# Optimization experiments

Measured on AMD Instinct MI355X. Metric: run time of the kernel, lower is better.

## Reference

```python
import jax, jax.numpy as jnp
import numpy as np

B, N, D, H, O, K, N_USER, C = 1, 4096, 64, 4, 64, 2, 4000, 2


def setup_inputs() -> dict:
    key = jax.random.key(0)
    ks = jax.random.split(key, 7)
    h = jax.random.normal(ks[0], (B, N, D), jnp.float32)
    # dense 0/1 adjacency per heterogeneous kind, with self-loops so no row is empty
    adj = jax.random.randint(ks[1], (K, B, N, N), 0, 2).astype(jnp.float32)
    hadj = jnp.maximum(adj, jnp.eye(N, dtype=jnp.float32))
    s = 1.0 / np.sqrt(D).astype(np.float32)
    w = jax.random.normal(ks[2], (K, H, D, O), jnp.float32) * s
    a_src = jax.random.normal(ks[3], (K, H, O, 1), jnp.float32) * (1.0 / np.sqrt(O).astype(np.float32))
    a_dst = jax.random.normal(ks[4], (K, H, O, 1), jnp.float32) * (1.0 / np.sqrt(O).astype(np.float32))
    fc_w = jax.random.normal(ks[5], (C, O * K), jnp.float32) * (1.0 / np.sqrt(O * K).astype(np.float32))
    fc_b = jnp.zeros((C,), jnp.float32)
    return {"h": h, "hadj": hadj, "w": w, "a_src": a_src, "a_dst": a_dst, "fc_w": fc_w, "fc_b": fc_b}


def _gat(h, adj, w_k, a_src_k, a_dst_k):
    # h: (B,N,D); adj: (B,N,N); w_k: (H,D,O); a_*: (H,O,1)
    h_prime = jnp.einsum('bnf,hfo->bhno', h, w_k)          # (B,H,N,O)
    t = jnp.tanh(h_prime)
    attn_src = jnp.einsum('bhno,hoi->bhni', t, a_src_k)    # (B,H,N,1)
    attn_dst = jnp.einsum('bhno,hoi->bhni', t, a_dst_k)    # (B,H,N,1)
    attn = attn_src + jnp.swapaxes(attn_dst, -1, -2)       # (B,H,N,N) broadcast add
    attn = jnp.where(attn >= 0, attn, 0.2 * attn)          # LeakyReLU(0.2)
    attn = jnp.where(adj[:, None] > 0, attn, -jnp.inf)     # dense mask
    attn = jax.nn.softmax(attn, axis=-1)                   # dropout is a no-op in eval
    out = jnp.einsum('bhnm,bhmo->bhno', attn, h_prime)     # (B,H,N,O)
    return out.mean(axis=1)                                # mean over heads -> (B,N,O)


def reference(h, hadj, w, a_src, a_dst, fc_w, fc_b):
    embs = []
    for k in range(K):  # small fixed loop over heterogeneous node kinds
        x = _gat(h, hadj[k], w[k], a_src[k], a_dst[k])
        embs.append(x[:, :N_USER])
    type_aware = jnp.concatenate(embs, axis=-1)            # (B, N_USER, K*O)
    logits = type_aware @ fc_w.T + fc_b                    # (B, N_USER, C)
    return jax.nn.log_softmax(logits, axis=-1)
```

## Files before the change

### kernel.cpp

```cpp
#include <hip/hip_runtime.h>
#include <math.h>

constexpr int KK = 2;
constexpr int HH = 4;
constexpr int NN = 4096;
constexpr int DD = 64;
constexpr int OO = 64;
constexpr int NU = 4000;
constexpr int CC = 2;
constexpr int JSPLIT = 8;
constexpr int JCHUNK = NN / JSPLIT;
constexpr float LOG2E = 1.44269504088896340736f;

typedef float vf4 __attribute__((ext_vector_type(4)));
typedef float vf2 __attribute__((ext_vector_type(2)));

__device__ __forceinline__ float fexp2(float x) {
#if __has_builtin(__builtin_amdgcn_exp2f)
  return __builtin_amdgcn_exp2f(x);
#else
  return exp2f(x);
#endif
}
__device__ __forceinline__ float frcp(float x) {
#if __has_builtin(__builtin_amdgcn_rcpf)
  return __builtin_amdgcn_rcpf(x);
#else
  return 1.0f / x;
#endif
}
__device__ __forceinline__ float ftanh(float x) {
  float e = fexp2(x * (2.0f * LOG2E));
  return 1.0f - 2.0f * frcp(e + 1.0f);
}

__global__ __launch_bounds__(256) void gat_phase1(
    const float* __restrict__ hsrc, const float* __restrict__ w,
    const float* __restrict__ a_src, const float* __restrict__ a_dst,
    const float* __restrict__ fc_w,
    float* __restrict__ Ap, float* __restrict__ A5p,
    float* __restrict__ Bp, float* __restrict__ B5p,
    float* __restrict__ G0p, float* __restrict__ G1p) {
  const int kh = blockIdx.y;
  const int k = kh >> 2;
  const int i0 = blockIdx.x * 64;
  const int tid = threadIdx.x;

  __shared__ float h_s[DD][68];
  __shared__ float w_s[DD][OO];
  __shared__ float part[4][64][17];

  {
    const vf4* wp = (const vf4*)(w + (size_t)kh * DD * OO);
    vf4* ws4 = (vf4*)w_s;
    for (int t = tid; t < DD * OO / 4; t += 256) ws4[t] = wp[t];
  }
  for (int t = tid; t < 1024; t += 256) {
    const int row = t >> 4;
    const int f4 = (t & 15) * 4;
    vf4 v = *(const vf4*)(hsrc + (size_t)(i0 + row) * DD + f4);
    h_s[f4 + 0][row] = v.x;
    h_s[f4 + 1][row] = v.y;
    h_s[f4 + 2][row] = v.z;
    h_s[f4 + 3][row] = v.w;
  }
  __syncthreads();

  const int og = tid & 15;
  const int rg = tid >> 4;
  const int o0 = og * 4;
  const int r0 = rg * 4;

  float hp[4][4];
#pragma unroll
  for (int j = 0; j < 4; ++j)
#pragma unroll
    for (int u = 0; u < 4; ++u) hp[j][u] = 0.0f;

#pragma unroll 8
  for (int f = 0; f < DD; ++f) {
    vf4 hv = *(const vf4*)&h_s[f][r0];
    vf4 wv = *(const vf4*)&w_s[f][o0];
    hp[0][0] = fmaf(hv.x, wv.x, hp[0][0]);
    hp[0][1] = fmaf(hv.x, wv.y, hp[0][1]);
    hp[0][2] = fmaf(hv.x, wv.z, hp[0][2]);
    hp[0][3] = fmaf(hv.x, wv.w, hp[0][3]);
    hp[1][0] = fmaf(hv.y, wv.x, hp[1][0]);
    hp[1][1] = fmaf(hv.y, wv.y, hp[1][1]);
    hp[1][2] = fmaf(hv.y, wv.z, hp[1][2]);
    hp[1][3] = fmaf(hv.y, wv.w, hp[1][3]);
    hp[2][0] = fmaf(hv.z, wv.x, hp[2][0]);
    hp[2][1] = fmaf(hv.z, wv.y, hp[2][1]);
    hp[2][2] = fmaf(hv.z, wv.z, hp[2][2]);
    hp[2][3] = fmaf(hv.z, wv.w, hp[2][3]);
    hp[3][0] = fmaf(hv.w, wv.x, hp[3][0]);
    hp[3][1] = fmaf(hv.w, wv.y, hp[3][1]);
    hp[3][2] = fmaf(hv.w, wv.z, hp[3][2]);
    hp[3][3] = fmaf(hv.w, wv.w, hp[3][3]);
  }

  float as[4], ad[4], f0[4], f1[4];
#pragma unroll
  for (int u = 0; u < 4; ++u) {
    as[u] = a_src[kh * OO + o0 + u];
    ad[u] = a_dst[kh * OO + o0 + u];
    f0[u] = fc_w[0 * (KK * OO) + k * OO + o0 + u];
    f1[u] = fc_w[1 * (KK * OO) + k * OO + o0 + u];
  }

#pragma unroll
  for (int j = 0; j < 4; ++j) {
    float sp = 0.0f, dp = 0.0f, g0 = 0.0f, g1 = 0.0f;
#pragma unroll
    for (int u = 0; u < 4; ++u) {
      float v = hp[j][u];
      float t = ftanh(v);
      sp = fmaf(t, as[u], sp);
      dp = fmaf(t, ad[u], dp);
      g0 = fmaf(v, f0[u], g0);
      g1 = fmaf(v, f1[u], g1);
    }
    part[0][r0 + j][og] = sp;
    part[1][r0 + j][og] = dp;
    part[2][r0 + j][og] = g0;
    part[3][r0 + j][og] = g1;
  }
  __syncthreads();

  {
    const int val = tid >> 6;
    const int j2 = tid & 63;
    const float* pr = &part[val][j2][0];
    vf4 s0 = *(const vf4*)(pr + 0);
    vf4 s1 = *(const vf4*)(pr + 4);
    vf4 s2 = *(const vf4*)(pr + 8);
    vf4 s3 = *(const vf4*)(pr + 12);
    vf4 t4 = s0 + s1 + s2 + s3;
    float sum = t4.x + t4.y + t4.z + t4.w;
    const size_t idx = (size_t)kh * NN + i0 + j2;
    if (val == 0) {
      float sp = sum * LOG2E;
      Ap[idx] = fexp2(sp);
      A5p[idx] = fexp2(0.2f * sp);
    } else if (val == 1) {
      float dp = sum * LOG2E;
      Bp[idx] = fexp2(dp);
      B5p[idx] = fexp2(0.2f * dp);
    } else if (val == 2) {
      G0p[idx] = sum;
    } else {
      G1p[idx] = sum;
    }
  }
}

__global__ __launch_bounds__(256) void gat_phase2(
    const float* __restrict__ adj, const float* __restrict__ Ap,
    const float* __restrict__ A5p, const float* __restrict__ Bp,
    const float* __restrict__ B5p, const float* __restrict__ G0p,
    const float* __restrict__ G1p, float* __restrict__ P) {
  const int k = blockIdx.y >> 3;
  const int chunk = blockIdx.y & 7;
  const int r0 = blockIdx.x * 16;
  const int tid = threadIdx.x;
  const int wave = tid >> 6;
  const int lane = tid & 63;
  const int row = lane & 15;
  const int jsub = lane >> 4;
  const int i = r0 + row;
  const int j0 = chunk * JCHUNK;

  __shared__ float lds[4][HH][JCHUNK];

  {
    const float* plane_src[4] = {Bp, B5p, G0p, G1p};
#pragma unroll
    for (int step = 0; step < 8; ++step) {
      const int wi = ((step & 1) << 8) | tid;
      const int h = wi >> 7;
      const int pos = (wi & 127) * 4;
      vf4 v = *(const vf4*)(plane_src[step >> 1] +
                            (size_t)(k * HH + h) * NN + j0 + pos);
      *(vf4*)&lds[step >> 1][h][pos] = v;
    }
  }

  const float* arow =
      adj + (size_t)k * NN * NN + (size_t)i * NN + j0 + jsub * 4;
  vf4 aj[8];
#pragma unroll
  for (int q = 0; q < 8; ++q)
    aj[q] = __builtin_nontemporal_load((const vf4*)(arow + (wave + q * 4) * 16));

  vf2 Apk[4], A5pk[4];
#pragma unroll
  for (int h = 0; h < 4; ++h) {
    const size_t ia = (size_t)(k * HH + h) * NN + i;
    float a = Ap[ia];
    float a5 = A5p[ia];
    Apk[h] = (vf2){a, a};
    A5pk[h] = (vf2){a5, a5};
  }

  vf2 l2[4], a02[4], a12[4];
#pragma unroll
  for (int h = 0; h < 4; ++h) {
    l2[h] = (vf2){0.0f, 0.0f};
    a02[h] = (vf2){0.0f, 0.0f};
    a12[h] = (vf2){0.0f, 0.0f};
  }

  __syncthreads();

#pragma unroll
  for (int s = 0; s < 8; ++s) {
    const int t = wave + s * 4;
    const vf4 av = aj[s];
    const vf2 av01 = (vf2){av.x, av.y};
    const vf2 av23 = (vf2){av.z, av.w};
    const int jl = t * 16 + jsub * 4;
#pragma unroll
    for (int h = 0; h < 4; ++h) {
      vf4 Bv = *(const vf4*)&lds[0][h][jl];
      vf4 B5v = *(const vf4*)&lds[1][h][jl];
      vf4 G0v = *(const vf4*)&lds[2][h][jl];
      vf4 G1v = *(const vf4*)&lds[3][h][jl];

      vf2 m01 = Apk[h] * (vf2){Bv.x, Bv.y};
      vf2 n01 = A5pk[h] * (vf2){B5v.x, B5v.y};
      vf2 e01 = (vf2){fmaxf(m01.x, n01.x), fmaxf(m01.y, n01.y)};
      vf2 pa01 = e01 * av01;
      l2[h] += pa01;
      a02[h] += pa01 * (vf2){G0v.x, G0v.y};
      a12[h] += pa01 * (vf2){G1v.x, G1v.y};

      vf2 m23 = Apk[h] * (vf2){Bv.z, Bv.w};
      vf2 n23 = A5pk[h] * (vf2){B5v.z, B5v.w};
      vf2 e23 = (vf2){fmaxf(m23.x, n23.x), fmaxf(m23.y, n23.y)};
      vf2 pa23 = e23 * av23;
      l2[h] += pa23;
      a02[h] += pa23 * (vf2){G0v.z, G0v.w};
      a12[h] += pa23 * (vf2){G1v.z, G1v.w};
    }
  }

  float l[4], a0[4], a1[4];
#pragma unroll
  for (int h = 0; h < 4; ++h) {
    l[h] = l2[h].x + l2[h].y;
    a0[h] = a02[h].x + a02[h].y;
    a1[h] = a12[h].x + a12[h].y;
  }
#pragma unroll
  for (int h = 0; h < 4; ++h) {
    l[h] += __shfl_xor(l[h], 16, 64);
    l[h] += __shfl_xor(l[h], 32, 64);
    a0[h] += __shfl_xor(a0[h], 16, 64);
    a0[h] += __shfl_xor(a0[h], 32, 64);
    a1[h] += __shfl_xor(a1[h], 16, 64);
    a1[h] += __shfl_xor(a1[h], 32, 64);
  }

  __shared__ float sred[4][12][16];
  if (lane < 16) {
#pragma unroll
    for (int h = 0; h < 4; ++h) {
      sred[wave][h * 3 + 0][row] = l[h];
      sred[wave][h * 3 + 1][row] = a0[h];
      sred[wave][h * 3 + 2][row] = a1[h];
    }
  }
  __syncthreads();
  if (tid < 192) {
    const int v = tid >> 4;
    const int rr = tid & 15;
    float sum =
        sred[0][v][rr] + sred[1][v][rr] + sred[2][v][rr] + sred[3][v][rr];
    const int h = v / 3, c = v % 3;
    size_t base =
        ((((size_t)(k * JSPLIT + chunk) * HH + h) * 3 + c)) * NU + (r0 + rr);
    P[base] = sum;
  }
}

__global__ __launch_bounds__(256) void gat_phase3(
    const float* __restrict__ P, const float* __restrict__ fc_b,
    float* __restrict__ out) {
  const int tid = threadIdx.x;
  const int il = tid & 31;
  const int g = tid >> 5;
  const int i = blockIdx.x * 32 + il;
  const int k = g >> 2, h = g & 3;

  float ls = 0.0f, a0 = 0.0f, a1 = 0.0f;
#pragma unroll
  for (int ch = 0; ch < JSPLIT; ++ch) {
    size_t b = (((size_t)(k * JSPLIT + ch) * HH + h) * 3) * NU + i;
    ls += P[b];
    a0 += P[b + NU];
    a1 += P[b + 2 * (size_t)NU];
  }
  float inv = 1.0f / ls;
  float p0 = 0.25f * a0 * inv;
  float p1 = 0.25f * a1 * inv;

  __shared__ float s0[8][33], s1[8][33];
  s0[g][il] = p0;
  s1[g][il] = p1;
  __syncthreads();

  if (tid < 32) {
    float l0 = fc_b[0], l1 = fc_b[1];
#pragma unroll
    for (int g2 = 0; g2 < 8; ++g2) {
      l0 += s0[g2][tid];
      l1 += s1[g2][tid];
    }
    const int io = blockIdx.x * 32 + tid;
    float m = fmaxf(l0, l1);
    float lse = m + logf(expf(l0 - m) + expf(l1 - m));
    vf2 r = {l0 - lse, l1 - lse};
    *(vf2*)(out + (size_t)io * CC) = r;
  }
}

extern "C" void kernel_launch(void* const* d_in, const int* in_sizes, int n_in,
                              void* d_out, int out_size, void* d_ws, size_t ws_size,
                              hipStream_t stream) {
  const float* hsrc  = (const float*)d_in[0];
  const float* hadj  = (const float*)d_in[1];
  const float* w     = (const float*)d_in[2];
  const float* a_src = (const float*)d_in[3];
  const float* a_dst = (const float*)d_in[4];
  const float* fc_w  = (const float*)d_in[5];
  const float* fc_b  = (const float*)d_in[6];
  float* out = (float*)d_out;

  char* ws = (char*)d_ws;
  float* Ap  = (float*)(ws + 0);
  float* A5p = (float*)(ws + 131072);
  float* Bp  = (float*)(ws + 262144);
  float* B5p = (float*)(ws + 393216);
  float* G0p = (float*)(ws + 524288);
  float* G1p = (float*)(ws + 655360);
  float* P   = (float*)(ws + 786432);

  dim3 g1(NN / 64, KK * HH);
  gat_phase1<<<g1, 256, 0, stream>>>(hsrc, w, a_src, a_dst, fc_w,
                                     Ap, A5p, Bp, B5p, G0p, G1p);
  dim3 g2(NU / 16, KK * JSPLIT);
  gat_phase2<<<g2, 256, 0, stream>>>(hadj, Ap, A5p, Bp, B5p, G0p, G1p, P);
  gat_phase3<<<NU / 32, 256, 0, stream>>>(P, fc_b, out);
}
```

Before: 229.3 us.

## Process two rows per thread in attention pass to reuse LDS node data

Phase 2 now gives each thread two adjacency rows (32 rows per block) while halving the column chunk (JSPLIT 8 to 16), so the grid keeps the same block count. Each LDS read of the per-column exp and feature planes is now shared by two rows, which halves LDS traffic per adjacency element. The packed two-wide float math becomes scalar fmaf. The partial-sum buffer P doubles in size, and phase 3 must reduce over twice as many chunks.

Measured after the change: 228.5 us. Within noise of the previous version (-0.3%).

```diff
diff --git a/kernel.cpp b/kernel.cpp
--- a/kernel.cpp
+++ b/kernel.cpp
@@ -8,7 +8,7 @@
 constexpr int OO = 64;
 constexpr int NU = 4000;
 constexpr int CC = 2;
-constexpr int JSPLIT = 8;
+constexpr int JSPLIT = 16;
 constexpr int JCHUNK = NN / JSPLIT;
 constexpr float LOG2E = 1.44269504088896340736f;
 
@@ -159,15 +159,16 @@
     const float* __restrict__ A5p, const float* __restrict__ Bp,
     const float* __restrict__ B5p, const float* __restrict__ G0p,
     const float* __restrict__ G1p, float* __restrict__ P) {
-  const int k = blockIdx.y >> 3;
-  const int chunk = blockIdx.y & 7;
-  const int r0 = blockIdx.x * 16;
+  const int k = blockIdx.y >> 4;
+  const int chunk = blockIdx.y & 15;
+  const int r0 = blockIdx.x * 32;
   const int tid = threadIdx.x;
   const int wave = tid >> 6;
   const int lane = tid & 63;
   const int row = lane & 15;
   const int jsub = lane >> 4;
-  const int i = r0 + row;
+  const int i0r = r0 + row;
+  const int i1r = r0 + 16 + row;
   const int j0 = chunk * JCHUNK;
 
   __shared__ float lds[4][HH][JCHUNK];
@@ -175,49 +176,52 @@
   {
     const float* plane_src[4] = {Bp, B5p, G0p, G1p};
 #pragma unroll
-    for (int step = 0; step < 8; ++step) {
-      const int wi = ((step & 1) << 8) | tid;
-      const int h = wi >> 7;
-      const int pos = (wi & 127) * 4;
-      vf4 v = *(const vf4*)(plane_src[step >> 1] +
+    for (int step = 0; step < 4; ++step) {
+      const int h = (tid >> 6) & 3;
+      const int pos = (tid & 63) * 4;
+      vf4 v = *(const vf4*)(plane_src[step] +
                             (size_t)(k * HH + h) * NN + j0 + pos);
-      *(vf4*)&lds[step >> 1][h][pos] = v;
-    }
-  }
-
-  const float* arow =
-      adj + (size_t)k * NN * NN + (size_t)i * NN + j0 + jsub * 4;
-  vf4 aj[8];
-#pragma unroll
-  for (int q = 0; q < 8; ++q)
-    aj[q] = __builtin_nontemporal_load((const vf4*)(arow + (wave + q * 4) * 16));
-
-  vf2 Apk[4], A5pk[4];
+      *(vf4*)&lds[step][h][pos] = v;
+    }
+  }
+
+  const size_t abase = (size_t)k * NN * NN + j0 + jsub * 4;
+  const float* ar0 = adj + abase + (size_t)i0r * NN;
+  const float* ar1 = adj + abase + (size_t)i1r * NN;
+  vf4 aj0[4], aj1[4];
+#pragma unroll
+  for (int q = 0; q < 4; ++q) {
+    aj0[q] = __builtin_nontemporal_load((const vf4*)(ar0 + (wave + q * 4) * 16));
+    aj1[q] = __builtin_nontemporal_load((const vf4*)(ar1 + (wave + q * 4) * 16));
+  }
+
+  float A0[4], A50[4], A1[4], A51[4];
 #pragma unroll
   for (int h = 0; h < 4; ++h) {
-    const size_t ia = (size_t)(k * HH + h) * NN + i;
-    float a = Ap[ia];
-    float a5 = A5p[ia];
-    Apk[h] = (vf2){a, a};
-    A5pk[h] = (vf2){a5, a5};
-  }
-
-  vf2 l2[4], a02[4], a12[4];
-#pragma unroll
-  for (int h = 0; h < 4; ++h) {
-    l2[h] = (vf2){0.0f, 0.0f};
-    a02[h] = (vf2){0.0f, 0.0f};
-    a12[h] = (vf2){0.0f, 0.0f};
-  }
-
-  __syncthreads();
-
-#pragma unroll
-  for (int s = 0; s < 8; ++s) {
+    const size_t pb = (size_t)(k * HH + h) * NN;
+    A0[h] = Ap[pb + i0r];
+    A50[h] = A5p[pb + i0r];
+    A1[h] = Ap[pb + i1r];
+    A51[h] = A5p[pb + i1r];
+  }
+
+  float l[2][4], a0[2][4], a1[2][4];
+#pragma unroll
+  for (int r = 0; r < 2; ++r)
+#pragma unroll
+    for (int h = 0; h < 4; ++h) {
+      l[r][h] = 0.0f;
+      a0[r][h] = 0.0f;
+      a1[r][h] = 0.0f;
+    }
+
+  __syncthreads();
+
+#pragma unroll
+  for (int s = 0; s < 4; ++s) {
     const int t = wave + s * 4;
-    const vf4 av = aj[s];
-    const vf2 av01 = (vf2){av.x, av.y};
-    const vf2 av23 = (vf2){av.z, av.w};
+    const vf4 av0 = aj0[s];
+    const vf4 av1 = aj1[s];
     const int jl = t * 16 + jsub * 4;
 #pragma unroll
     for (int h = 0; h < 4; ++h) {
@@ -225,61 +229,59 @@
       vf4 B5v = *(const vf4*)&lds[1][h][jl];
       vf4 G0v = *(const vf4*)&lds[2][h][jl];
       vf4 G1v = *(const vf4*)&lds[3][h][jl];
-
-      vf2 m01 = Apk[h] * (vf2){Bv.x, Bv.y};
-      vf2 n01 = A5pk[h] * (vf2){B5v.x, B5v.y};
-      vf2 e01 = (vf2){fmaxf(m01.x, n01.x), fmaxf(m01.y, n01.y)};
-      vf2 pa01 = e01 * av01;
-      l2[h] += pa01;
-      a02[h] += pa01 * (vf2){G0v.x, G0v.y};
-      a12[h] += pa01 * (vf2){G1v.x, G1v.y};
-
-      vf2 m23 = Apk[h] * (vf2){Bv.z, Bv.w};
-      vf2 n23 = A5pk[h] * (vf2){B5v.z, B5v.w};
-      vf2 e23 = (vf2){fmaxf(m23.x, n23.x), fmaxf(m23.y, n23.y)};
-      vf2 pa23 = e23 * av23;
-      l2[h] += pa23;
-      a02[h] += pa23 * (vf2){G0v.z, G0v.w};
-      a12[h] += pa23 * (vf2){G1v.z, G1v.w};
-    }
-  }
-
-  float l[4], a0[4], a1[4];
-#pragma unroll
-  for (int h = 0; h < 4; ++h) {
-    l[h] = l2[h].x + l2[h].y;
-    a0[h] = a02[h].x + a02[h].y;
-    a1[h] = a12[h].x + a12[h].y;
-  }
-#pragma unroll
-  for (int h = 0; h < 4; ++h) {
-    l[h] += __shfl_xor(l[h], 16, 64);
-    l[h] += __shfl_xor(l[h], 32, 64);
-    a0[h] += __shfl_xor(a0[h], 16, 64);
-    a0[h] += __shfl_xor(a0[h], 32, 64);
-    a1[h] += __shfl_xor(a1[h], 16, 64);
-    a1[h] += __shfl_xor(a1[h], 32, 64);
-  }
-
-  __shared__ float sred[4][12][16];
-  if (lane < 16) {
+#pragma unroll
+      for (int jj = 0; jj < 4; ++jj) {
+        const float b = Bv[jj], b5 = B5v[jj];
+        const float g0 = G0v[jj], g1 = G1v[jj];
+        float e0 = fmaxf(A0[h] * b, A50[h] * b5);
+        float pa0 = e0 * av0[jj];
+        l[0][h] += pa0;
+        a0[0][h] = fmaf(pa0, g0, a0[0][h]);
+        a1[0][h] = fmaf(pa0, g1, a1[0][h]);
+        float e1 = fmaxf(A1[h] * b, A51[h] * b5);
+        float pa1 = e1 * av1[jj];
+        l[1][h] += pa1;
+        a0[1][h] = fmaf(pa1, g0, a0[1][h]);
+        a1[1][h] = fmaf(pa1, g1, a1[1][h]);
+      }
+    }
+  }
+
+#pragma unroll
+  for (int r = 0; r < 2; ++r)
 #pragma unroll
     for (int h = 0; h < 4; ++h) {
-      sred[wave][h * 3 + 0][row] = l[h];
-      sred[wave][h * 3 + 1][row] = a0[h];
-      sred[wave][h * 3 + 2][row] = a1[h];
+      l[r][h] += __shfl_xor(l[r][h], 16, 64);
+      l[r][h] += __shfl_xor(l[r][h], 32, 64);
+      a0[r][h] += __shfl_xor(a0[r][h], 16, 64);
+      a0[r][h] += __shfl_xor(a0[r][h], 32, 64);
+      a1[r][h] += __shfl_xor(a1[r][h], 16, 64);
+      a1[r][h] += __shfl_xor(a1[r][h], 32, 64);
+    }
+
+  __shared__ float sred[4][12][32];
+  if (lane < 32) {
+    const int half = lane >> 4;
+#pragma unroll
+    for (int h = 0; h < 4; ++h) {
+      sred[wave][h * 3 + 0][row + 16 * half] = l[half][h];
+      sred[wave][h * 3 + 1][row + 16 * half] = a0[half][h];
+      sred[wave][h * 3 + 2][row + 16 * half] = a1[half][h];
     }
   }
   __syncthreads();
   if (tid < 192) {
     const int v = tid >> 4;
-    const int rr = tid & 15;
-    float sum =
-        sred[0][v][rr] + sred[1][v][rr] + sred[2][v][rr] + sred[3][v][rr];
     const int h = v / 3, c = v % 3;
-    size_t base =
-        ((((size_t)(k * JSPLIT + chunk) * HH + h) * 3 + c)) * NU + (r0 + rr);
-    P[base] = sum;
+    const size_t pbase =
+        ((((size_t)(k * JSPLIT + chunk) * HH + h) * 3 + c)) * NU + r0;
+#pragma unroll
+    for (int half = 0; half < 2; ++half) {
+      const int rr = (tid & 15) + 16 * half;
+      float sum =
+          sred[0][v][rr] + sred[1][v][rr] + sred[2][v][rr] + sred[3][v][rr];
+      P[pbase + rr] = sum;
+    }
   }
 }
 
@@ -348,7 +350,7 @@
   dim3 g1(NN / 64, KK * HH);
   gat_phase1<<<g1, 256, 0, stream>>>(hsrc, w, a_src, a_dst, fc_w,
                                      Ap, A5p, Bp, B5p, G0p, G1p);
-  dim3 g2(NU / 16, KK * JSPLIT);
+  dim3 g2(NU / 32, KK * JSPLIT);
   gat_phase2<<<g2, 256, 0, stream>>>(hadj, Ap, A5p, Bp, B5p, G0p, G1p, P);
   gat_phase3<<<NU / 32, 256, 0, stream>>>(P, fc_b, out);
 }
```
